# Kernel tuning notes

Measured on AMD Instinct MI355X. Metric: run time of the kernel, lower is better.

The kernel has to match this reference:

```python
import jax, jax.numpy as jnp
import numpy as np

B, S, D = 8, 2048, 1024


def setup_inputs() -> dict:
    key = jax.random.key(0)
    ks = jax.random.split(key, 10)
    s = 0.02
    x = jax.random.normal(ks[0], (B, S, D), dtype=jnp.float32)
    # causal boolean mask [B, S, S]
    mask = jnp.broadcast_to(jnp.tril(jnp.ones((S, S), dtype=bool)), (B, S, S))
    Wq = jax.random.normal(ks[1], (D, D), dtype=jnp.float32) * s
    bq = jax.random.normal(ks[2], (D,), dtype=jnp.float32) * s
    Wk = jax.random.normal(ks[3], (D, D), dtype=jnp.float32) * s
    bk = jax.random.normal(ks[4], (D,), dtype=jnp.float32) * s
    Wv = jax.random.normal(ks[5], (D, D), dtype=jnp.float32) * s
    bv = jax.random.normal(ks[6], (D,), dtype=jnp.float32) * s
    Wo = jax.random.normal(ks[7], (D, D), dtype=jnp.float32) * s
    bo = jax.random.normal(ks[8], (D,), dtype=jnp.float32) * s
    return {"x": x, "mask": mask, "Wq": Wq, "bq": bq, "Wk": Wk, "bk": bk,
            "Wv": Wv, "bv": bv, "Wo": Wo, "bo": bo}


def reference(x, mask, Wq, bq, Wk, bk, Wv, bv, Wo, bo):
    # no cache -> cache_len = 0, full x/mask used; dropout=0.0 (identity)
    d_k = x.shape[-1]
    q = jnp.einsum('bsd,ed->bse', x, Wq) + bq
    k = jnp.einsum('bsd,ed->bse', x, Wk) + bk  # computed but unused (original bug)
    v = jnp.einsum('bsd,ed->bse', x, Wv) + bv
    # NOTE: original code uses q @ v^T (not k) - reproduced faithfully
    scores = jnp.einsum('bqd,bkd->bqk', q, v) / jnp.sqrt(jnp.float32(d_k))
    scores = jnp.where(mask, scores, jnp.float32(-jnp.inf))
    attn = jax.nn.softmax(scores, axis=-1)
    ctx = jnp.einsum('bqk,bkd->bqd', attn, v)
    out = jnp.einsum('bsd,ed->bse', ctx, Wo) + bo
    return out
```

## Files before the change

kernel.cpp:

```cpp
#include <hip/hip_runtime.h>

typedef unsigned short u16;
typedef __attribute__((ext_vector_type(8))) unsigned short u16x8;
typedef __bf16 bf16x8 __attribute__((ext_vector_type(8)));
typedef float f32x4 __attribute__((ext_vector_type(4)));

__device__ __forceinline__ u16 f2b(float f) {
    unsigned u = __float_as_uint(f);
    u += 0x7fffu + ((u >> 16) & 1u);
    return (u16)(u >> 16);
}
__device__ __forceinline__ float b2f(u16 h) {
    return __uint_as_float(((unsigned)h) << 16);
}

__device__ __forceinline__ void async_copy16(const void* g, void* l) {
    __builtin_amdgcn_global_load_lds(
        (const __attribute__((address_space(1))) unsigned int*)g,
        (__attribute__((address_space(3))) unsigned int*)l,
        16, 0, 0);
}

__global__ __launch_bounds__(256) void cast_kernel(const float* __restrict__ in,
                                                   u16* __restrict__ out, long n) {
    long i0 = ((long)blockIdx.x * 256 + threadIdx.x) * 8;
    long stride = (long)gridDim.x * 256 * 8;
    for (long i = i0; i < n; i += stride) {
        float4 a = *(const float4*)(in + i);
        float4 b = *(const float4*)(in + i + 4);
        u16x8 o;
        o[0] = f2b(a.x); o[1] = f2b(a.y); o[2] = f2b(a.z); o[3] = f2b(a.w);
        o[4] = f2b(b.x); o[5] = f2b(b.y); o[6] = f2b(b.z); o[7] = f2b(b.w);
        *(u16x8*)(out + i) = o;
    }
}

__global__ __launch_bounds__(256) void transpose_kernel(const u16* __restrict__ in,
                                                        u16* __restrict__ out,
                                                        int rows, int cols) {
    __shared__ u16 tile[32][33];
    long base = (long)blockIdx.z * rows * cols;
    const u16* I = in + base;
    u16* O = out + base;
    int r0 = blockIdx.y * 32, c0 = blockIdx.x * 32;
    int tx = threadIdx.x, ty = threadIdx.y;
    #pragma unroll
    for (int j = ty; j < 32; j += 8)
        tile[j][tx] = I[(long)(r0 + j) * cols + c0 + tx];
    __syncthreads();
    #pragma unroll
    for (int j = ty; j < 32; j += 8)
        O[(long)(c0 + j) * rows + r0 + tx] = tile[tx][j];
}

__global__ __launch_bounds__(256) void softmax_kernel(u16* __restrict__ Sc) {
    const int SS = 2048;
    long row = blockIdx.x;
    int q = (int)(row & (SS - 1));
    int L = q + 1;
    int Klim = ((q >> 7) + 1) << 7;
    u16* p = Sc + row * SS;
    int tid = threadIdx.x;

    float m = -1e30f;
    for (int i = tid; i < L; i += 256) m = fmaxf(m, b2f(p[i]));
    #pragma unroll
    for (int o = 32; o > 0; o >>= 1) m = fmaxf(m, __shfl_xor(m, o));
    __shared__ float redm[4];
    if ((tid & 63) == 0) redm[tid >> 6] = m;
    __syncthreads();
    m = fmaxf(fmaxf(redm[0], redm[1]), fmaxf(redm[2], redm[3]));

    float s = 0.f;
    for (int i = tid; i < L; i += 256) s += __expf(b2f(p[i]) - m);
    #pragma unroll
    for (int o = 32; o > 0; o >>= 1) s += __shfl_xor(s, o);
    __shared__ float reds[4];
    if ((tid & 63) == 0) reds[tid >> 6] = s;
    __syncthreads();
    s = reds[0] + reds[1] + reds[2] + reds[3];
    float inv = 1.f / s;

    for (int i = tid; i < Klim; i += 256) {
        float v = (i < L) ? __expf(b2f(p[i]) - m) * inv : 0.f;
        p[i] = f2b(v);
    }
}

template<typename OUTT, bool BIAS, bool CSKIP, bool KLIM>
__global__ __launch_bounds__(256, 2)
void gemm_bt(const u16* __restrict__ Aall, const u16* __restrict__ Ball,
             const float* __restrict__ bias, OUTT* __restrict__ Call,
             int M, int N, int K, float scale, long sA, long sB, long sC) {
    const int bz = blockIdx.z;
    const u16* A = Aall + (long)bz * sA;
    const u16* Bm = Ball + (long)bz * sB;
    OUTT* C = Call + (long)bz * sC;
    const int bm = blockIdx.y, bn = blockIdx.x;
    if (CSKIP && bn > bm) return;
    int Keff = K;
    if (KLIM) { int kl = (bm + 1) * 128; Keff = kl < K ? kl : K; }

    __shared__ u16 As[128 * 32];
    __shared__ u16 Bs[128 * 32];

    const int tid = threadIdx.x;
    const int lane = tid & 63;
    const int w = tid >> 6;
    const int wr = (w >> 1) * 64;
    const int wc = (w & 1) * 64;

    const int fr = lane & 15;
    const int fk = (lane >> 4) * 8;

    f32x4 acc[4][4] = {};

    const long rowA0 = (long)bm * 128;
    const long colB0 = (long)bn * 128;

    for (int k0 = 0; k0 < Keff; k0 += 32) {
        #pragma unroll
        for (int rr = 0; rr < 2; ++rr) {
            int c = rr * 256 + tid;
            const u16* gA = A + (rowA0 + (c >> 2)) * K + k0 + (c & 3) * 8;
            async_copy16(gA, As + (rr * 256 + w * 64) * 8);
            const u16* gB = Bm + (colB0 + (c >> 2)) * K + k0 + (c & 3) * 8;
            async_copy16(gB, Bs + (rr * 256 + w * 64) * 8);
        }
        __syncthreads();

        bf16x8 af[4], bfv[4];
        #pragma unroll
        for (int m = 0; m < 4; ++m)
            af[m] = *(const bf16x8*)(As + (wr + m * 16 + fr) * 32 + fk);
        #pragma unroll
        for (int n = 0; n < 4; ++n)
            bfv[n] = *(const bf16x8*)(Bs + (wc + n * 16 + fr) * 32 + fk);
        #pragma unroll
        for (int m = 0; m < 4; ++m)
            #pragma unroll
            for (int n = 0; n < 4; ++n)
                acc[m][n] = __builtin_amdgcn_mfma_f32_16x16x32_bf16(af[m], bfv[n], acc[m][n], 0, 0, 0);
        __syncthreads();
    }

    const int crow0 = (int)rowA0 + wr + (lane >> 4) * 4;
    const int ccol0 = (int)colB0 + wc + (lane & 15);
    #pragma unroll
    for (int m = 0; m < 4; ++m) {
        #pragma unroll
        for (int n = 0; n < 4; ++n) {
            int col = ccol0 + n * 16;
            float bvv = BIAS ? bias[col] : 0.f;
            #pragma unroll
            for (int j = 0; j < 4; ++j) {
                int rowi = crow0 + m * 16 + j;
                float v = acc[m][n][j] * scale + bvv;
                if constexpr (sizeof(OUTT) == 2) {
                    C[(long)rowi * N + col] = (OUTT)f2b(v);
                } else {
                    C[(long)rowi * N + col] = v;
                }
            }
        }
    }
}

extern "C" void kernel_launch(void* const* d_in, const int* in_sizes, int n_in,
                              void* d_out, int out_size, void* d_ws, size_t ws_size,
                              hipStream_t stream) {
    const float* x  = (const float*)d_in[0];
    const float* Wq = (const float*)d_in[2];
    const float* bq = (const float*)d_in[3];
    const float* Wv = (const float*)d_in[6];
    const float* bv = (const float*)d_in[7];
    const float* Wo = (const float*)d_in[8];
    const float* bo = (const float*)d_in[9];
    float* out = (float*)d_out;

    const long B = 8, S = 2048, D = 1024;
    const long MS = B * S;

    char* p = (char*)d_ws;
    u16* xb  = (u16*)p; p += MS * D * 2;
    u16* Wqb = (u16*)p; p += D * D * 2;
    u16* Wvb = (u16*)p; p += D * D * 2;
    u16* Wob = (u16*)p; p += D * D * 2;
    u16* Qb  = (u16*)p; p += MS * D * 2;
    u16* Vb  = (u16*)p; p += MS * D * 2;
    u16* Sb  = (u16*)p; p += B * S * S * 2;
    u16* ctxb = xb;
    u16* Vtb  = Qb;

    cast_kernel<<<4096, 256, 0, stream>>>(x, xb, MS * D);
    cast_kernel<<<512, 256, 0, stream>>>(Wq, Wqb, D * D);
    cast_kernel<<<512, 256, 0, stream>>>(Wv, Wvb, D * D);
    cast_kernel<<<512, 256, 0, stream>>>(Wo, Wob, D * D);

    dim3 gproj(D / 128, MS / 128, 1);
    gemm_bt<u16, true, false, false><<<gproj, 256, 0, stream>>>(
        xb, Wqb, bq, Qb, (int)MS, (int)D, (int)D, 1.0f, 0, 0, 0);
    gemm_bt<u16, true, false, false><<<gproj, 256, 0, stream>>>(
        xb, Wvb, bv, Vb, (int)MS, (int)D, (int)D, 1.0f, 0, 0, 0);

    dim3 gsc(S / 128, S / 128, B);
    gemm_bt<u16, false, true, false><<<gsc, 256, 0, stream>>>(
        Qb, Vb, nullptr, Sb, (int)S, (int)S, (int)D, 0.03125f, S * D, S * D, S * S);

    softmax_kernel<<<MS, 256, 0, stream>>>(Sb);

    dim3 gtr(D / 32, S / 32, B);
    transpose_kernel<<<gtr, dim3(32, 8), 0, stream>>>(Vb, Vtb, (int)S, (int)D);

    dim3 gpv(D / 128, S / 128, B);
    gemm_bt<u16, false, false, true><<<gpv, 256, 0, stream>>>(
        Sb, Vtb, nullptr, ctxb, (int)S, (int)D, (int)S, 1.0f, S * S, D * S, S * D);

    gemm_bt<float, true, false, false><<<gproj, 256, 0, stream>>>(
        ctxb, Wob, bo, out, (int)MS, (int)D, (int)D, 1.0f, 0, 0, 0);
}
```

Before: 607.9 us.

## Replace 128x128 GEMM with 256x256 tile, 8-wave, double-buffered swizzled pipeline

Replaces the simple 128x128, BK=32 GEMM with a 256x256-tile, BK=64 kernel of 512 threads. It uses 128 KB of dynamic LDS split into two buffers and staged in quarter-tile halves. LDS addresses are XOR-swizzled to avoid bank conflicts, and global-to-LDS async loads are interleaved with four MFMA phases guarded by explicit waitcnt, barriers and setprio. The softmax zero-fill and the PV K-limit are widened to 256 granularity to match the new tile. The aim is higher data reuse and overlap of loads with MFMA, at the cost of one workgroup per CU and coarser causal skipping.

Result: faster. 559.0 us (-8.0%).

```diff
diff --git a/kernel.cpp b/kernel.cpp
--- a/kernel.cpp
+++ b/kernel.cpp
@@ -20,6 +20,8 @@
         (__attribute__((address_space(3))) unsigned int*)l,
         16, 0, 0);
 }
+
+__device__ __forceinline__ int swz(int x) { return x ^ (((x >> 9) & 1) << 5); }
 
 __global__ __launch_bounds__(256) void cast_kernel(const float* __restrict__ in,
                                                    u16* __restrict__ out, long n) {
@@ -58,7 +60,7 @@
     long row = blockIdx.x;
     int q = (int)(row & (SS - 1));
     int L = q + 1;
-    int Klim = ((q >> 7) + 1) << 7;
+    int Klim = ((q >> 8) + 1) << 8;
     u16* p = Sc + row * SS;
     int tid = threadIdx.x;
 
@@ -88,78 +90,171 @@
 }
 
 template<typename OUTT, bool BIAS, bool CSKIP, bool KLIM>
-__global__ __launch_bounds__(256, 2)
-void gemm_bt(const u16* __restrict__ Aall, const u16* __restrict__ Ball,
+__global__ __launch_bounds__(512)
+void gemm256(const u16* __restrict__ Aall, const u16* __restrict__ Ball,
              const float* __restrict__ bias, OUTT* __restrict__ Call,
              int M, int N, int K, float scale, long sA, long sB, long sC) {
     const int bz = blockIdx.z;
     const u16* A = Aall + (long)bz * sA;
-    const u16* Bm = Ball + (long)bz * sB;
+    const u16* B = Ball + (long)bz * sB;
     OUTT* C = Call + (long)bz * sC;
     const int bm = blockIdx.y, bn = blockIdx.x;
     if (CSKIP && bn > bm) return;
     int Keff = K;
-    if (KLIM) { int kl = (bm + 1) * 128; Keff = kl < K ? kl : K; }
-
-    __shared__ u16 As[128 * 32];
-    __shared__ u16 Bs[128 * 32];
+    if (KLIM) { int kl = (bm + 1) * 256; Keff = kl < K ? kl : K; }
+    const int NT = Keff >> 6;
+
+    extern __shared__ __align__(16) char lds[];
 
     const int tid = threadIdx.x;
     const int lane = tid & 63;
     const int w = tid >> 6;
-    const int wr = (w >> 1) * 64;
-    const int wc = (w & 1) * 64;
-
-    const int fr = lane & 15;
-    const int fk = (lane >> 4) * 8;
-
-    f32x4 acc[4][4] = {};
-
-    const long rowA0 = (long)bm * 128;
-    const long colB0 = (long)bn * 128;
-
-    for (int k0 = 0; k0 < Keff; k0 += 32) {
-        #pragma unroll
-        for (int rr = 0; rr < 2; ++rr) {
-            int c = rr * 256 + tid;
-            const u16* gA = A + (rowA0 + (c >> 2)) * K + k0 + (c & 3) * 8;
-            async_copy16(gA, As + (rr * 256 + w * 64) * 8);
-            const u16* gB = Bm + (colB0 + (c >> 2)) * K + k0 + (c & 3) * 8;
-            async_copy16(gB, Bs + (rr * 256 + w * 64) * 8);
+    const int wm = w >> 2, wn = w & 3;
+    const int fr = lane & 15, hi = lane >> 4;
+    const int axor = ((fr >> 2) & 1) << 5;
+
+    const long rowA0 = (long)bm * 256;
+    const long rowB0 = (long)bn * 256;
+
+    auto stage_half = [&](const u16* mat, long gr0, int k0, char* region) {
+        #pragma unroll
+        for (int rd = 0; rd < 2; ++rd) {
+            int pb = rd * 8192 + w * 1024;
+            int p = pb + lane * 16;
+            int L = swz(p);
+            const u16* src = mat + (gr0 + (L >> 7)) * (long)K + k0 + ((L & 127) >> 1);
+            async_copy16(src, region + pb);
         }
-        __syncthreads();
-
-        bf16x8 af[4], bfv[4];
-        #pragma unroll
-        for (int m = 0; m < 4; ++m)
-            af[m] = *(const bf16x8*)(As + (wr + m * 16 + fr) * 32 + fk);
-        #pragma unroll
-        for (int n = 0; n < 4; ++n)
-            bfv[n] = *(const bf16x8*)(Bs + (wc + n * 16 + fr) * 32 + fk);
-        #pragma unroll
-        for (int m = 0; m < 4; ++m)
-            #pragma unroll
-            for (int n = 0; n < 4; ++n)
-                acc[m][n] = __builtin_amdgcn_mfma_f32_16x16x32_bf16(af[m], bfv[n], acc[m][n], 0, 0, 0);
-        __syncthreads();
-    }
-
-    const int crow0 = (int)rowA0 + wr + (lane >> 4) * 4;
-    const int ccol0 = (int)colB0 + wc + (lane & 15);
-    #pragma unroll
-    for (int m = 0; m < 4; ++m) {
+    };
+
+    f32x4 acc[8][4] = {};
+    bf16x8 a[4][2], b0[2][2], b1[2][2];
+
+    char* bufp0 = lds;
+    char* bufp1 = lds + 65536;
+
+    stage_half(A, rowA0,       0, bufp0 + 0 * 16384);
+    stage_half(B, rowB0,       0, bufp0 + 2 * 16384);
+    stage_half(B, rowB0 + 128, 0, bufp0 + 3 * 16384);
+    stage_half(A, rowA0 + 128, 0, bufp0 + 1 * 16384);
+    asm volatile("s_waitcnt vmcnt(4)" ::: "memory");
+    if (1 < NT) {
+        stage_half(A, rowA0,       64, bufp1 + 0 * 16384);
+        stage_half(B, rowB0,       64, bufp1 + 2 * 16384);
+        stage_half(B, rowB0 + 128, 64, bufp1 + 3 * 16384);
+    }
+    asm volatile("s_waitcnt vmcnt(6)" ::: "memory");
+    __builtin_amdgcn_s_barrier();
+
+    const int abase = (wm * 64 + fr) * 128 + hi * 16;
+    const int bbase = (wn * 32 + fr) * 128 + hi * 16;
+
+    for (int u = 0; u < NT; ++u) {
+        char* bufp  = (u & 1) ? bufp1 : bufp0;
+        char* obufp = (u & 1) ? bufp0 : bufp1;
+
+        #pragma unroll
+        for (int m = 0; m < 4; ++m)
+            #pragma unroll
+            for (int kk = 0; kk < 2; ++kk)
+                a[m][kk] = *(const bf16x8*)(bufp + 0 * 16384 + ((abase + m * 2048 + kk * 64) ^ axor));
+        #pragma unroll
+        for (int nl = 0; nl < 2; ++nl)
+            #pragma unroll
+            for (int kk = 0; kk < 2; ++kk)
+                b0[nl][kk] = *(const bf16x8*)(bufp + 2 * 16384 + ((bbase + nl * 2048 + kk * 64) ^ axor));
+        if (u + 1 < NT)
+            stage_half(A, rowA0 + 128, (u + 1) * 64, obufp + 1 * 16384);
+        asm volatile("s_waitcnt lgkmcnt(8)" ::: "memory");
+        __builtin_amdgcn_s_barrier();
+        asm volatile("s_waitcnt lgkmcnt(0)" ::: "memory");
+        __builtin_amdgcn_sched_barrier(0);
+        __builtin_amdgcn_s_setprio(1);
+        #pragma unroll
+        for (int m = 0; m < 4; ++m)
+            #pragma unroll
+            for (int nl = 0; nl < 2; ++nl)
+                #pragma unroll
+                for (int kk = 0; kk < 2; ++kk)
+                    acc[m][nl] = __builtin_amdgcn_mfma_f32_16x16x32_bf16(a[m][kk], b0[nl][kk], acc[m][nl], 0, 0, 0);
+        __builtin_amdgcn_s_setprio(0);
+        __builtin_amdgcn_s_barrier();
+
+        #pragma unroll
+        for (int nl = 0; nl < 2; ++nl)
+            #pragma unroll
+            for (int kk = 0; kk < 2; ++kk)
+                b1[nl][kk] = *(const bf16x8*)(bufp + 3 * 16384 + ((bbase + nl * 2048 + kk * 64) ^ axor));
+        if (u + 2 < NT)
+            stage_half(A, rowA0, (u + 2) * 64, bufp + 0 * 16384);
+        __builtin_amdgcn_s_barrier();
+        asm volatile("s_waitcnt lgkmcnt(0)" ::: "memory");
+        __builtin_amdgcn_sched_barrier(0);
+        __builtin_amdgcn_s_setprio(1);
+        #pragma unroll
+        for (int m = 0; m < 4; ++m)
+            #pragma unroll
+            for (int nl = 0; nl < 2; ++nl)
+                #pragma unroll
+                for (int kk = 0; kk < 2; ++kk)
+                    acc[m][2 + nl] = __builtin_amdgcn_mfma_f32_16x16x32_bf16(a[m][kk], b1[nl][kk], acc[m][2 + nl], 0, 0, 0);
+        __builtin_amdgcn_s_setprio(0);
+        __builtin_amdgcn_s_barrier();
+
+        #pragma unroll
+        for (int m = 0; m < 4; ++m)
+            #pragma unroll
+            for (int kk = 0; kk < 2; ++kk)
+                a[m][kk] = *(const bf16x8*)(bufp + 1 * 16384 + ((abase + m * 2048 + kk * 64) ^ axor));
+        if (u + 2 < NT)
+            stage_half(B, rowB0, (u + 2) * 64, bufp + 2 * 16384);
+        __builtin_amdgcn_s_barrier();
+        asm volatile("s_waitcnt lgkmcnt(0)" ::: "memory");
+        __builtin_amdgcn_sched_barrier(0);
+        __builtin_amdgcn_s_setprio(1);
+        #pragma unroll
+        for (int m = 0; m < 4; ++m)
+            #pragma unroll
+            for (int nl = 0; nl < 2; ++nl)
+                #pragma unroll
+                for (int kk = 0; kk < 2; ++kk)
+                    acc[4 + m][2 + nl] = __builtin_amdgcn_mfma_f32_16x16x32_bf16(a[m][kk], b1[nl][kk], acc[4 + m][2 + nl], 0, 0, 0);
+        __builtin_amdgcn_s_setprio(0);
+        __builtin_amdgcn_s_barrier();
+
+        if (u + 2 < NT)
+            stage_half(B, rowB0 + 128, (u + 2) * 64, bufp + 3 * 16384);
+        __builtin_amdgcn_s_barrier();
+        __builtin_amdgcn_s_setprio(1);
+        #pragma unroll
+        for (int m = 0; m < 4; ++m)
+            #pragma unroll
+            for (int nl = 0; nl < 2; ++nl)
+                #pragma unroll
+                for (int kk = 0; kk < 2; ++kk)
+                    acc[4 + m][nl] = __builtin_amdgcn_mfma_f32_16x16x32_bf16(a[m][kk], b0[nl][kk], acc[4 + m][nl], 0, 0, 0);
+        __builtin_amdgcn_s_setprio(0);
+        if (u < NT - 2) { asm volatile("s_waitcnt vmcnt(6)" ::: "memory"); }
+        else            { asm volatile("s_waitcnt vmcnt(0)" ::: "memory"); }
+        __builtin_amdgcn_s_barrier();
+    }
+
+    #pragma unroll
+    for (int m = 0; m < 8; ++m) {
+        int rl = (m < 4) ? (wm * 64 + m * 16) : (128 + wm * 64 + (m - 4) * 16);
+        long grow = rowA0 + rl + hi * 4;
         #pragma unroll
         for (int n = 0; n < 4; ++n) {
-            int col = ccol0 + n * 16;
-            float bvv = BIAS ? bias[col] : 0.f;
+            int cl = (n < 2) ? (wn * 32 + n * 16) : (128 + wn * 32 + (n - 2) * 16);
+            long gcol = rowB0 + cl + fr;
+            float bvv = BIAS ? bias[gcol] : 0.f;
             #pragma unroll
             for (int j = 0; j < 4; ++j) {
-                int rowi = crow0 + m * 16 + j;
                 float v = acc[m][n][j] * scale + bvv;
                 if constexpr (sizeof(OUTT) == 2) {
-                    C[(long)rowi * N + col] = (OUTT)f2b(v);
+                    C[(grow + j) * N + gcol] = (OUTT)f2b(v);
                 } else {
-                    C[(long)rowi * N + col] = v;
+                    C[(grow + j) * N + gcol] = v;
                 }
             }
         }
@@ -169,6 +264,7 @@
 extern "C" void kernel_launch(void* const* d_in, const int* in_sizes, int n_in,
                               void* d_out, int out_size, void* d_ws, size_t ws_size,
                               hipStream_t stream) {
+    (void)in_sizes; (void)n_in; (void)out_size; (void)ws_size;
     const float* x  = (const float*)d_in[0];
     const float* Wq = (const float*)d_in[2];
     const float* bq = (const float*)d_in[3];
@@ -192,19 +288,29 @@
     u16* ctxb = xb;
     u16* Vtb  = Qb;
 
+    const int SMEM = 131072;
+    (void)hipFuncSetAttribute((const void*)gemm256<u16, true, false, false>,
+                              hipFuncAttributeMaxDynamicSharedMemorySize, SMEM);
+    (void)hipFuncSetAttribute((const void*)gemm256<u16, false, true, false>,
+                              hipFuncAttributeMaxDynamicSharedMemorySize, SMEM);
+    (void)hipFuncSetAttribute((const void*)gemm256<u16, false, false, true>,
+                              hipFuncAttributeMaxDynamicSharedMemorySize, SMEM);
+    (void)hipFuncSetAttribute((const void*)gemm256<float, true, false, false>,
+                              hipFuncAttributeMaxDynamicSharedMemorySize, SMEM);
+
     cast_kernel<<<4096, 256, 0, stream>>>(x, xb, MS * D);
     cast_kernel<<<512, 256, 0, stream>>>(Wq, Wqb, D * D);
     cast_kernel<<<512, 256, 0, stream>>>(Wv, Wvb, D * D);
     cast_kernel<<<512, 256, 0, stream>>>(Wo, Wob, D * D);
 
-    dim3 gproj(D / 128, MS / 128, 1);
-    gemm_bt<u16, true, false, false><<<gproj, 256, 0, stream>>>(
+    dim3 gproj(D / 256, MS / 256, 1);
+    gemm256<u16, true, false, false><<<gproj, 512, SMEM, stream>>>(
         xb, Wqb, bq, Qb, (int)MS, (int)D, (int)D, 1.0f, 0, 0, 0);
-    gemm_bt<u16, true, false, false><<<gproj, 256, 0, stream>>>(
+    gemm256<u16, true, false, false><<<gproj, 512, SMEM, stream>>>(
         xb, Wvb, bv, Vb, (int)MS, (int)D, (int)D, 1.0f, 0, 0, 0);
 
-    dim3 gsc(S / 128, S / 128, B);
-    gemm_bt<u16, false, true, false><<<gsc, 256, 0, stream>>>(
+    dim3 gsc(S / 256, S / 256, B);
+    gemm256<u16, false, true, false><<<gsc, 512, SMEM, stream>>>(
         Qb, Vb, nullptr, Sb, (int)S, (int)S, (int)D, 0.03125f, S * D, S * D, S * S);
 
     softmax_kernel<<<MS, 256, 0, stream>>>(Sb);
@@ -212,10 +318,10 @@
     dim3 gtr(D / 32, S / 32, B);
     transpose_kernel<<<gtr, dim3(32, 8), 0, stream>>>(Vb, Vtb, (int)S, (int)D);
 
-    dim3 gpv(D / 128, S / 128, B);
-    gemm_bt<u16, false, false, true><<<gpv, 256, 0, stream>>>(
+    dim3 gpv(D / 256, S / 256, B);
+    gemm256<u16, false, false, true><<<gpv, 512, SMEM, stream>>>(
         Sb, Vtb, nullptr, ctxb, (int)S, (int)D, (int)S, 1.0f, S * S, D * S, S * D);
 
-    gemm_bt<float, true, false, false><<<gproj, 256, 0, stream>>>(
+    gemm256<float, true, false, false><<<gproj, 512, SMEM, stream>>>(
         ctxb, Wob, bo, out, (int)MS, (int)D, (int)D, 1.0f, 0, 0, 0);
 }
```
